# Performance work log

Measured on AMD Instinct MI355X. Metric: run time of the kernel, lower is better.

## Reference

```python
import jax, jax.numpy as jnp
import numpy as np

IN_DIM = 784   # 28*28
OUT_DIM = 16
NUM = 5        # grid intervals
K = 3          # spline order
HEADS = 10


def _make_grid():
    # pykan extended grid: linspace(-1,1,NUM+1) extended by K knots on each side
    h = 2.0 / NUM
    pts = np.arange(-K, NUM + K + 1, dtype=np.float32) * h - 1.0  # [NUM+2K+1]=12
    return jnp.asarray(np.broadcast_to(pts, (IN_DIM, pts.shape[0])))


def setup_inputs() -> dict:
    key = jax.random.key(0)
    ks = jax.random.split(key, 6)
    B = 16384
    x = jax.random.normal(ks[0], (B, 1, 28, 28), jnp.float32)
    grid = _make_grid()                                             # [784,12] (buffer)
    coef = jax.random.normal(ks[1], (HEADS, IN_DIM, OUT_DIM, NUM + K), jnp.float32) * 0.1
    scale_base = jax.random.normal(ks[2], (HEADS, IN_DIM, OUT_DIM), jnp.float32) * 0.1
    scale_sp = jnp.ones((HEADS, IN_DIM, OUT_DIM), jnp.float32)
    mask = jnp.ones((HEADS, IN_DIM, OUT_DIM), jnp.float32)
    w1 = jax.random.normal(ks[3], (HEADS, 8, OUT_DIM), jnp.float32) / np.sqrt(OUT_DIM)
    b1 = jnp.zeros((HEADS, 8), jnp.float32)
    w2 = jax.random.normal(ks[4], (HEADS, 1, 8), jnp.float32) / np.sqrt(8.0)
    b2 = jnp.zeros((HEADS, 1), jnp.float32)
    return dict(x=x, grid=grid, coef=coef, scale_base=scale_base, scale_sp=scale_sp,
                mask=mask, w1=w1, b1=b1, w2=w2, b2=b2)


def _b_spline(x, grid, k):
    # x: [B, D], grid: [D, G] -> bases [B, D, G-k-1] (Cox-de Boor recursion, pykan B_batch)
    xg = x[:, :, None]
    g = grid[None]
    B = ((xg >= g[:, :, :-1]) & (xg < g[:, :, 1:])).astype(x.dtype)
    for p in range(1, k + 1):
        left = (xg - g[:, :, :-(p + 1)]) / (g[:, :, p:-1] - g[:, :, :-(p + 1)])
        right = (g[:, :, p + 1:] - xg) / (g[:, :, p + 1:] - g[:, :, 1:-p])
        B = left * B[:, :, :-1] + right * B[:, :, 1:]
    return jnp.nan_to_num(B)


def reference(x, grid, coef, scale_base, scale_sp, mask, w1, b1, w2, b2):
    xf = x.reshape(x.shape[0], -1)                  # [B, 784]
    Bsp = _b_spline(xf, grid, K)                    # [B, 784, NUM+K]
    # KANLayer: y = sum_d mask*(scale_base*silu(x) + scale_sp*spline). Sum over d is
    # linear, so fold (scale_sp*mask) into coef to avoid the [B,H,784,16] intermediate.
    eff_coef = coef * (scale_sp * mask)[..., None]  # [H, 784, 16, NUM+K]
    y_sp = jnp.einsum('bdg,hdog->bho', Bsp, eff_coef)
    y_base = jnp.einsum('bd,hdo->bho', jax.nn.silu(xf), scale_base * mask)
    y = jnp.tanh(y_base + y_sp)                     # [B, H, 16] (nn.Tanh)
    h1 = jnp.tanh(jnp.einsum('bho,hpo->bhp', y, w1) + b1[None])   # Linear(16,8)+Tanh
    out = jnp.einsum('bhp,hqp->bhq', h1, w2) + b2[None]           # Linear(8,1)
    return out[..., 0]                              # concat of 10 heads -> [B, 10]
```

## Files before the change

### kernel.cpp

```cpp
#include <hip/hip_runtime.h>

#define IN_DIM 784
#define NDB 25
#define NUNITS (NDB*9)
#define BATCH 16384
#define NOUTC 160
#define HEADS 10
#define KSPLIT 4
#define MROWS 128
#define ROWB 584
#define CHUNKB (MROWS*ROWB)

typedef __attribute__((ext_vector_type(8))) short bf16x8;
typedef __attribute__((ext_vector_type(4))) float f32x4;

__device__ __forceinline__ unsigned short f2bf(float f) {
    unsigned u = __builtin_bit_cast(unsigned, f);
    unsigned r = 0x7FFFu + ((u >> 16) & 1u);
    return (unsigned short)((u + r) >> 16);
}

__global__ void k_wprep(const float* __restrict__ coef, const float* __restrict__ scale_base,
                        const float* __restrict__ scale_sp, const float* __restrict__ mask,
                        unsigned short* __restrict__ Wp) {
    int tid = blockIdx.x * blockDim.x + threadIdx.x;
    if (tid >= NUNITS * 32 * NOUTC) return;
    int frag = tid >> 9;
    int rem  = tid & 511;
    int l = rem >> 3, j = rem & 7;
    int kc = frag / 10, nt = frag - kc * 10;
    int db = kc / 9, c = kc - db * 9;
    int kk = ((l >> 4) << 3) + j;
    int d = db * 32 + kk;
    int n = nt * 16 + (l & 15);
    float v = 0.f;
    if (d < IN_DIM) {
        int h = n >> 4, o = n & 15;
        size_t base = ((size_t)h * IN_DIM + d) * 16 + o;
        float m = mask[base];
        v = (c == 0) ? scale_base[base] * m
                     : coef[base * 8 + (c - 1)] * scale_sp[base] * m * 0.16666667f;
    }
    Wp[tid] = f2bf(v);
}

__global__ void __launch_bounds__(512, 4) k_fused(const float* __restrict__ x,
                                                  const float* __restrict__ gridp,
                                                  const unsigned short* __restrict__ Wp,
                                                  float* __restrict__ part) {
    __shared__ char ldsb[CHUNKB];
    const int tid = threadIdx.x;
    const int l = tid & 63, wid = tid >> 6;
    const int rr = l & 15, q = l >> 4;
    const int rp = wid >> 1, nh = wid & 1;
    const int sd = tid & 31, srg = tid >> 5;
    const int row0g = blockIdx.x * MROWS;
    const int y = blockIdx.y;
    const int db0 = (y * NDB) >> 2, db1 = ((y + 1) * NDB) >> 2;

    const float g0 = gridp[0];
    const float ih = 1.f / (gridp[1] - g0);
    const float nihg0 = -g0 * ih;

    f32x4 acc[2][5];
    #pragma unroll
    for (int rg = 0; rg < 2; ++rg)
        #pragma unroll
        for (int i = 0; i < 5; ++i) acc[rg][i] = (f32x4){0.f, 0.f, 0.f, 0.f};

    const char* wpb = (const char*)Wp;
    float xv[8];

    auto loadX = [&](int db) {
        const int d = db * 32 + sd;
        const int dc = d < IN_DIM ? d : IN_DIM - 1;
        const float* xp = x + (size_t)(row0g + srg) * IN_DIM + dc;
        #pragma unroll
        for (int it = 0; it < 8; ++it) xv[it] = xp[(size_t)it * 16 * IN_DIM];
    };

    auto evalScatter = [&]() {
        char* rb0 = ldsb + srg * ROWB + sd * 2;
        #pragma unroll
        for (int it = 0; it < 8; ++it) {
            const float v = xv[it];
            const float u = fmaf(v, ih, nihg0);
            const float fm = floorf(u);
            const int m = (int)fm;
            const float t = u - fm;
            const float t2 = t * t;
            const float w0 = t2 * t;
            const float w1 = fmaf(fmaf(fmaf(-3.f, t, 3.f), t, 3.f), t, 1.f);
            const float w2 = fmaf(fmaf(3.f, t, -6.f) * t, t, 4.f);
            const float omt = 1.f - t;
            const float w3 = omt * omt * omt;
            const float den = 1.f + __expf(-v);
            float inv; asm("v_rcp_f32 %0, %1" : "=v"(inv) : "v"(den));
            const float sil = v * inv;
            unsigned p01, p23, ps;
            asm("v_cvt_pk_bf16_f32 %0, %1, %2" : "=v"(p01) : "v"(w0), "v"(w1));
            asm("v_cvt_pk_bf16_f32 %0, %1, %2" : "=v"(p23) : "v"(w2), "v"(w3));
            asm("v_cvt_pk_bf16_f32 %0, %1, %2" : "=v"(ps)  : "v"(sil), "v"(sil));
            const unsigned h1 = p01 >> 16, h3 = p23 >> 16;
            char* rb = rb0 + it * 16 * ROWB;
            *(unsigned short*)rb = (unsigned short)ps;
            #pragma unroll
            for (int s = 0; s < 8; ++s) {
                const int ms = m - s;
                unsigned wv = 0u;
                if (s <= 3) {
                    const unsigned wsel = (s == 0) ? p01 : (s == 1) ? h1 : (s == 2) ? p23 : h3;
                    wv = ((unsigned)ms <= 7u) ? wsel : 0u;
                }
                *(unsigned short*)(rb + (((unsigned)ms & 7u) << 6) + 64) = (unsigned short)wv;
            }
        }
    };

    loadX(db0);
    #pragma unroll 1
    for (int db = db0; db < db1; ++db) {
        __syncthreads();
        evalScatter();
        if (db + 1 < db1) loadX(db + 1);
        __syncthreads();

        const char* arow = ldsb + (rp * 32 + rr) * ROWB + q * 16;
        const char* bb = wpb + (size_t)db * 92160 + nh * 5120 + l * 16;
        bf16x8 bn[5];
        #pragma unroll
        for (int nt = 0; nt < 5; ++nt) bn[nt] = *(const bf16x8*)(bb + nt * 1024);
        #pragma unroll
        for (int c = 0; c < 9; ++c) {
            bf16x8 bc[5];
            #pragma unroll
            for (int nt = 0; nt < 5; ++nt) bc[nt] = bn[nt];
            if (c < 8) {
                const char* bnx = bb + (c + 1) * 10240;
                #pragma unroll
                for (int nt = 0; nt < 5; ++nt) bn[nt] = *(const bf16x8*)(bnx + nt * 1024);
            }
            const bf16x8 a0 = *(const bf16x8*)(arow + c * 64);
            const bf16x8 a1 = *(const bf16x8*)(arow + 16 * ROWB + c * 64);
            #pragma unroll
            for (int nt = 0; nt < 5; ++nt) {
                acc[0][nt] = __builtin_amdgcn_mfma_f32_16x16x32_bf16(a0, bc[nt], acc[0][nt], 0, 0, 0);
                acc[1][nt] = __builtin_amdgcn_mfma_f32_16x16x32_bf16(a1, bc[nt], acc[1][nt], 0, 0, 0);
            }
        }
    }

    float* pp = part + (size_t)y * BATCH * NOUTC;
    #pragma unroll
    for (int rg = 0; rg < 2; ++rg) {
        #pragma unroll
        for (int ntl = 0; ntl < 5; ++ntl) {
            const int col = (nh * 5 + ntl) * 16 + rr;
            #pragma unroll
            for (int ii = 0; ii < 4; ++ii)
                pp[(size_t)(row0g + (rp * 2 + rg) * 16 + q * 4 + ii) * NOUTC + col] = acc[rg][ntl][ii];
        }
    }
}

__global__ void k_epi(const float* __restrict__ part, const float* __restrict__ w1,
                      const float* __restrict__ b1, const float* __restrict__ w2,
                      const float* __restrict__ b2, float* __restrict__ out) {
    int t = blockIdx.x * blockDim.x + threadIdx.x;
    if (t >= BATCH * HEADS) return;
    int b = t / HEADS;
    int h = t - b * HEADS;
    const f32x4* P = (const f32x4*)part;
    const int vbase = b * (NOUTC / 4) + h * 4;
    float y[16];
    #pragma unroll
    for (int c4 = 0; c4 < 4; ++c4) {
        f32x4 v = P[vbase + c4];
        #pragma unroll
        for (int s = 1; s < KSPLIT; ++s) {
            f32x4 v2 = P[(size_t)s * BATCH * (NOUTC / 4) + vbase + c4];
            v.x += v2.x; v.y += v2.y; v.z += v2.z; v.w += v2.w;
        }
        y[c4 * 4 + 0] = tanhf(v.x); y[c4 * 4 + 1] = tanhf(v.y);
        y[c4 * 4 + 2] = tanhf(v.z); y[c4 * 4 + 3] = tanhf(v.w);
    }
    float oacc = b2[h];
    #pragma unroll
    for (int p = 0; p < 8; ++p) {
        float a = b1[h * 8 + p];
        const float* wr = w1 + ((size_t)h * 8 + p) * 16;
        #pragma unroll
        for (int o = 0; o < 16; ++o) a = fmaf(y[o], wr[o], a);
        oacc = fmaf(tanhf(a), w2[h * 8 + p], oacc);
    }
    out[t] = oacc;
}

extern "C" void kernel_launch(void* const* d_in, const int* in_sizes, int n_in,
                              void* d_out, int out_size, void* d_ws, size_t ws_size,
                              hipStream_t stream) {
    const float* x          = (const float*)d_in[0];
    const float* gridp      = (const float*)d_in[1];
    const float* coef       = (const float*)d_in[2];
    const float* scale_base = (const float*)d_in[3];
    const float* scale_sp   = (const float*)d_in[4];
    const float* mask       = (const float*)d_in[5];
    const float* w1         = (const float*)d_in[6];
    const float* b1         = (const float*)d_in[7];
    const float* w2         = (const float*)d_in[8];
    const float* b2         = (const float*)d_in[9];
    float* out = (float*)d_out;

    char* ws = (char*)d_ws;
    float* part        = (float*)ws;
    unsigned short* Wp = (unsigned short*)(ws + 41943040);

    k_wprep<<<dim3((NUNITS * 32 * NOUTC + 255) / 256), dim3(256), 0, stream>>>(coef, scale_base, scale_sp, mask, Wp);
    k_fused<<<dim3(BATCH / MROWS, KSPLIT), dim3(512), 0, stream>>>(x, gridp, Wp, part);
    k_epi  <<<dim3((BATCH * HEADS + 255) / 256), dim3(256), 0, stream>>>(part, w1, b1, w2, b2, out);
}
```

Baseline: 121.5 us.

## Build spline A-fragments in registers and stream weights to LDS with 32x32 MFMA

The fused kernel no longer scatters B-spline bases into a large LDS row buffer. Each lane now loads its own x values, keeps packed bf16 basis weights and interval indices in registers, and builds the A operand for each of the 9 coefficient slots on the fly. Weight tiles are double-buffered into LDS through global_load_lds, and the MFMA shape changes from 16x16x32 to 32x32x16 with 256-thread blocks. The K split goes from 4 to 5 (5 d-blocks each), so the weight prep layout and workspace offset change to match. This removes the LDS scatter and per-chunk barrier traffic, at the cost of more VALU work to select fragments and a sync on every weight unit.

```diff
diff --git a/kernel.cpp b/kernel.cpp
--- a/kernel.cpp
+++ b/kernel.cpp
@@ -6,18 +6,25 @@
 #define BATCH 16384
 #define NOUTC 160
 #define HEADS 10
-#define KSPLIT 4
-#define MROWS 128
-#define ROWB 584
-#define CHUNKB (MROWS*ROWB)
+#define KSPLIT 5
+#define DBPY 5
+#define UNITB 10240
 
 typedef __attribute__((ext_vector_type(8))) short bf16x8;
 typedef __attribute__((ext_vector_type(4))) float f32x4;
+typedef __attribute__((ext_vector_type(16))) float f32x16;
+typedef __attribute__((ext_vector_type(4))) unsigned int u32x4;
 
 __device__ __forceinline__ unsigned short f2bf(float f) {
     unsigned u = __builtin_bit_cast(unsigned, f);
     unsigned r = 0x7FFFu + ((u >> 16) & 1u);
     return (unsigned short)((u + r) >> 16);
+}
+
+__device__ __forceinline__ void gload_lds16(const void* g, void* s) {
+    __builtin_amdgcn_global_load_lds(
+        (const __attribute__((address_space(1))) unsigned int*)g,
+        (__attribute__((address_space(3))) unsigned int*)s, 16, 0, 0);
 }
 
 __global__ void k_wprep(const float* __restrict__ coef, const float* __restrict__ scale_base,
@@ -28,11 +35,13 @@
     int frag = tid >> 9;
     int rem  = tid & 511;
     int l = rem >> 3, j = rem & 7;
-    int kc = frag / 10, nt = frag - kc * 10;
+    int nt = frag % 5;
+    int t2 = frag / 5;
+    int kh = t2 & 1;
+    int kc = t2 >> 1;
     int db = kc / 9, c = kc - db * 9;
-    int kk = ((l >> 4) << 3) + j;
-    int d = db * 32 + kk;
-    int n = nt * 16 + (l & 15);
+    int d = db * 32 + kh * 16 + ((l >> 5) << 3) + j;
+    int n = nt * 32 + (l & 31);
     float v = 0.f;
     if (d < IN_DIM) {
         int h = n >> 4, o = n & 15;
@@ -44,121 +53,162 @@
     Wp[tid] = f2bf(v);
 }
 
-__global__ void __launch_bounds__(512, 4) k_fused(const float* __restrict__ x,
+__global__ void __launch_bounds__(256, 3) k_fused(const float* __restrict__ x,
                                                   const float* __restrict__ gridp,
                                                   const unsigned short* __restrict__ Wp,
                                                   float* __restrict__ part) {
-    __shared__ char ldsb[CHUNKB];
+    __shared__ __attribute__((aligned(16))) char ldsB[2][UNITB];
     const int tid = threadIdx.x;
     const int l = tid & 63, wid = tid >> 6;
-    const int rr = l & 15, q = l >> 4;
-    const int rp = wid >> 1, nh = wid & 1;
-    const int sd = tid & 31, srg = tid >> 5;
-    const int row0g = blockIdx.x * MROWS;
+    const int la = l & 31, lb = l >> 5;
+    const int row0 = blockIdx.x * 128 + wid * 32 + la;
     const int y = blockIdx.y;
-    const int db0 = (y * NDB) >> 2, db1 = ((y + 1) * NDB) >> 2;
+    const int db0 = y * DBPY, db1 = db0 + DBPY;
 
     const float g0 = gridp[0];
     const float ih = 1.f / (gridp[1] - g0);
     const float nihg0 = -g0 * ih;
 
-    f32x4 acc[2][5];
-    #pragma unroll
-    for (int rg = 0; rg < 2; ++rg)
-        #pragma unroll
-        for (int i = 0; i < 5; ++i) acc[rg][i] = (f32x4){0.f, 0.f, 0.f, 0.f};
-
+    f32x16 acc[5];
+    #pragma unroll
+    for (int nt = 0; nt < 5; ++nt)
+        #pragma unroll
+        for (int j = 0; j < 16; ++j) acc[nt][j] = 0.f;
+
+    const float* xrow = x + (size_t)row0 * IN_DIM;
     const char* wpb = (const char*)Wp;
-    float xv[8];
-
-    auto loadX = [&](int db) {
-        const int d = db * 32 + sd;
-        const int dc = d < IN_DIM ? d : IN_DIM - 1;
-        const float* xp = x + (size_t)(row0g + srg) * IN_DIM + dc;
-        #pragma unroll
-        for (int it = 0; it < 8; ++it) xv[it] = xp[(size_t)it * 16 * IN_DIM];
-    };
-
-    auto evalScatter = [&]() {
-        char* rb0 = ldsb + srg * ROWB + sd * 2;
-        #pragma unroll
-        for (int it = 0; it < 8; ++it) {
-            const float v = xv[it];
-            const float u = fmaf(v, ih, nihg0);
+
+    unsigned long long wp[2][8];
+    unsigned mp[2][2];
+    unsigned sf[2][4];
+    f32x4 xq[2][2];
+
+    auto xload = [&](int db) {
+        #pragma unroll
+        for (int kh = 0; kh < 2; ++kh) {
+            if (db * 32 + kh * 16 < IN_DIM) {
+                const int d0 = db * 32 + kh * 16 + lb * 8;
+                xq[kh][0] = *(const f32x4*)(xrow + d0);
+                xq[kh][1] = *(const f32x4*)(xrow + d0 + 4);
+            }
+        }
+    };
+
+    auto evalkh = [&](int kh) {
+        float sil8[8];
+        unsigned m0 = 0u, m1 = 0u;
+        #pragma unroll
+        for (int jj = 0; jj < 8; ++jj) {
+            const float xv = (jj < 4) ? xq[kh][0][jj] : xq[kh][1][jj - 4];
+            const float u = fmaf(xv, ih, nihg0);
             const float fm = floorf(u);
-            const int m = (int)fm;
+            int m = (int)fm;
+            m = m < -8 ? -8 : (m > 24 ? 24 : m);
             const float t = u - fm;
-            const float t2 = t * t;
-            const float w0 = t2 * t;
+            const float w0 = t * t * t;
             const float w1 = fmaf(fmaf(fmaf(-3.f, t, 3.f), t, 3.f), t, 1.f);
             const float w2 = fmaf(fmaf(3.f, t, -6.f) * t, t, 4.f);
             const float omt = 1.f - t;
             const float w3 = omt * omt * omt;
-            const float den = 1.f + __expf(-v);
+            const float den = 1.f + __expf(-xv);
             float inv; asm("v_rcp_f32 %0, %1" : "=v"(inv) : "v"(den));
-            const float sil = v * inv;
-            unsigned p01, p23, ps;
+            sil8[jj] = xv * inv;
+            unsigned p01, p23;
             asm("v_cvt_pk_bf16_f32 %0, %1, %2" : "=v"(p01) : "v"(w0), "v"(w1));
             asm("v_cvt_pk_bf16_f32 %0, %1, %2" : "=v"(p23) : "v"(w2), "v"(w3));
-            asm("v_cvt_pk_bf16_f32 %0, %1, %2" : "=v"(ps)  : "v"(sil), "v"(sil));
-            const unsigned h1 = p01 >> 16, h3 = p23 >> 16;
-            char* rb = rb0 + it * 16 * ROWB;
-            *(unsigned short*)rb = (unsigned short)ps;
+            wp[kh][jj] = (unsigned long long)p01 | ((unsigned long long)p23 << 32);
+            const unsigned mb = (unsigned)(m + 8);
+            if (jj < 4) m0 |= mb << (jj * 8); else m1 |= mb << ((jj - 4) * 8);
+        }
+        mp[kh][0] = m0; mp[kh][1] = m1;
+        #pragma unroll
+        for (int pr = 0; pr < 4; ++pr) {
+            unsigned ps;
+            asm("v_cvt_pk_bf16_f32 %0, %1, %2" : "=v"(ps) : "v"(sil8[2*pr]), "v"(sil8[2*pr+1]));
+            sf[kh][pr] = ps;
+        }
+    };
+
+    auto buildA = [&](int kh, int c) -> bf16x8 {
+        u32x4 fw;
+        if (c == 0) {
+            fw = (u32x4){sf[kh][0], sf[kh][1], sf[kh][2], sf[kh][3]};
+        } else {
+            const unsigned sub = (unsigned)(7 + c);
             #pragma unroll
-            for (int s = 0; s < 8; ++s) {
-                const int ms = m - s;
-                unsigned wv = 0u;
-                if (s <= 3) {
-                    const unsigned wsel = (s == 0) ? p01 : (s == 1) ? h1 : (s == 2) ? p23 : h3;
-                    wv = ((unsigned)ms <= 7u) ? wsel : 0u;
+            for (int pr = 0; pr < 4; ++pr) {
+                unsigned lo, hi;
+                {
+                    const int j = 2 * pr;
+                    const unsigned stored = (mp[kh][j >> 2] >> ((j & 3) * 8)) & 0xFFu;
+                    const unsigned idx = stored - sub;
+                    const unsigned amt = (idx << 4) & 63u;
+                    lo = (unsigned)(wp[kh][j] >> amt) & 0xFFFFu;
+                    lo = (idx <= 3u) ? lo : 0u;
                 }
-                *(unsigned short*)(rb + (((unsigned)ms & 7u) << 6) + 64) = (unsigned short)wv;
+                {
+                    const int j = 2 * pr + 1;
+                    const unsigned stored = (mp[kh][j >> 2] >> ((j & 3) * 8)) & 0xFFu;
+                    const unsigned idx = stored - sub;
+                    const unsigned amt = (idx << 4) & 63u;
+                    hi = (unsigned)(wp[kh][j] >> amt) & 0xFFFFu;
+                    hi = (idx <= 3u) ? hi : 0u;
+                }
+                fw[pr] = lo | (hi << 16);
             }
         }
-    };
-
-    loadX(db0);
+        return __builtin_bit_cast(bf16x8, fw);
+    };
+
+    auto stage = [&](int pb, int db, int c) {
+        const char* src = wpb + (size_t)(db * 9 + c) * UNITB + (size_t)l * 16;
+        char* dst = &ldsB[pb][0];
+        gload_lds16(src + (size_t)wid * 1024,       dst + wid * 1024);
+        gload_lds16(src + (size_t)(wid + 4) * 1024, dst + (wid + 4) * 1024);
+        if (wid < 2)
+            gload_lds16(src + (size_t)(wid + 8) * 1024, dst + (wid + 8) * 1024);
+    };
+
+    xload(db0);
+    stage(0, db0, 0);
+    __syncthreads();
+
+    int p = 0;
     #pragma unroll 1
-    for (int db = db0; db < db1; ++db) {
+    for (int u = 0; u < DBPY * 9; ++u) {
+        const int db = db0 + u / 9;
+        const int c  = u - 9 * (u / 9);
+        if (u + 1 < DBPY * 9)
+            stage(p ^ 1, db0 + (u + 1) / 9, (u + 1) % 9);
+        if (c == 0) {
+            evalkh(0);
+            evalkh(1);
+            if (db + 1 < db1) xload(db + 1);
+        }
+        #pragma unroll
+        for (int kh = 0; kh < 2; ++kh) {
+            if (kh == 0 || db < 24) {
+                const bf16x8 a = buildA(kh, c);
+                const char* bp = &ldsB[p][kh * 5120] + l * 16;
+                #pragma unroll
+                for (int nt = 0; nt < 5; ++nt) {
+                    const bf16x8 b = *(const bf16x8*)(bp + nt * 1024);
+                    acc[nt] = __builtin_amdgcn_mfma_f32_32x32x16_bf16(a, b, acc[nt], 0, 0, 0);
+                }
+            }
+        }
         __syncthreads();
-        evalScatter();
-        if (db + 1 < db1) loadX(db + 1);
-        __syncthreads();
-
-        const char* arow = ldsb + (rp * 32 + rr) * ROWB + q * 16;
-        const char* bb = wpb + (size_t)db * 92160 + nh * 5120 + l * 16;
-        bf16x8 bn[5];
-        #pragma unroll
-        for (int nt = 0; nt < 5; ++nt) bn[nt] = *(const bf16x8*)(bb + nt * 1024);
-        #pragma unroll
-        for (int c = 0; c < 9; ++c) {
-            bf16x8 bc[5];
-            #pragma unroll
-            for (int nt = 0; nt < 5; ++nt) bc[nt] = bn[nt];
-            if (c < 8) {
-                const char* bnx = bb + (c + 1) * 10240;
-                #pragma unroll
-                for (int nt = 0; nt < 5; ++nt) bn[nt] = *(const bf16x8*)(bnx + nt * 1024);
-            }
-            const bf16x8 a0 = *(const bf16x8*)(arow + c * 64);
-            const bf16x8 a1 = *(const bf16x8*)(arow + 16 * ROWB + c * 64);
-            #pragma unroll
-            for (int nt = 0; nt < 5; ++nt) {
-                acc[0][nt] = __builtin_amdgcn_mfma_f32_16x16x32_bf16(a0, bc[nt], acc[0][nt], 0, 0, 0);
-                acc[1][nt] = __builtin_amdgcn_mfma_f32_16x16x32_bf16(a1, bc[nt], acc[1][nt], 0, 0, 0);
-            }
-        }
+        p ^= 1;
     }
 
     float* pp = part + (size_t)y * BATCH * NOUTC;
-    #pragma unroll
-    for (int rg = 0; rg < 2; ++rg) {
-        #pragma unroll
-        for (int ntl = 0; ntl < 5; ++ntl) {
-            const int col = (nh * 5 + ntl) * 16 + rr;
-            #pragma unroll
-            for (int ii = 0; ii < 4; ++ii)
-                pp[(size_t)(row0g + (rp * 2 + rg) * 16 + q * 4 + ii) * NOUTC + col] = acc[rg][ntl][ii];
+    const int rowb = blockIdx.x * 128 + wid * 32;
+    #pragma unroll
+    for (int nt = 0; nt < 5; ++nt) {
+        #pragma unroll
+        for (int r = 0; r < 16; ++r) {
+            const int rl = (r & 3) + 8 * (r >> 2) + 4 * lb;
+            pp[(size_t)(rowb + rl) * NOUTC + nt * 32 + la] = acc[nt][r];
         }
     }
 }
@@ -213,9 +263,9 @@
 
     char* ws = (char*)d_ws;
     float* part        = (float*)ws;
-    unsigned short* Wp = (unsigned short*)(ws + 41943040);
+    unsigned short* Wp = (unsigned short*)(ws + 52428800);
 
     k_wprep<<<dim3((NUNITS * 32 * NOUTC + 255) / 256), dim3(256), 0, stream>>>(coef, scale_base, scale_sp, mask, Wp);
-    k_fused<<<dim3(BATCH / MROWS, KSPLIT), dim3(512), 0, stream>>>(x, gridp, Wp, part);
+    k_fused<<<dim3(BATCH / 128, KSPLIT), dim3(256), 0, stream>>>(x, gridp, Wp, part);
     k_epi  <<<dim3((BATCH * HEADS + 255) / 256), dim3(256), 0, stream>>>(part, w1, b1, w2, b2, out);
 }
```

After: 137.1 us. 12.8% more time.
